# Kernel optimization log

Measured on AMD Instinct MI355X. Metric: run time of the kernel, lower is better.

## Reference

```python
import jax, jax.numpy as jnp
import numpy as np

SAMPLES = 8    # batch of sets
N = 1024       # set size == rows of the permutation-closed index matrix
K = 16         # number of distinct weight-sharing groups
M = N // K     # columns per group per row (rectangular splits)
CI = 128       # channels_in
CO = 256       # channels_out


def setup_inputs() -> dict:
    key = jax.random.key(0)
    kx, kw = jax.random.split(key)
    x = jax.random.normal(kx, (SAMPLES, N, CI), dtype=jnp.float32)
    # weightParameter: [k, channels_out, channels_in]
    W = jax.random.normal(kw, (K, CO, CI), dtype=jnp.float32)
    # Rebuild the circulant group structure that __init__ derives from
    # running_weight_matrix: row j of `indices` is roll(base, j), so the
    # columns of group g in row j are (pos_g + j) mod N.
    base = np.repeat(np.arange(K), M)                      # indices row 0, [N]
    pos = np.stack([np.where(base == g)[0] for g in range(K)])  # [K, M]
    splits = (pos[:, None, :] + np.arange(N)[None, :, None]) % N  # [K, N, M]
    return {"x": x, "W": W, "splits": jnp.asarray(splits, jnp.int32)}


def reference(x, W, splits):
    # sum-pool branch: result = sum_g ( sum_m x[:, splits[g]] ) @ W[g].T
    def body(acc, group):
        w, sp = group                      # w: [CO, CI], sp: [N, M]
        pooled = x[:, sp].sum(axis=2)      # gather [S, N, M, CI] -> [S, N, CI]
        return acc + jnp.einsum('snc,oc->sno', pooled, w), None

    init = jnp.zeros((x.shape[0], splits.shape[1], W.shape[1]), dtype=x.dtype)
    out, _ = jax.lax.scan(body, init, (W, splits))
    return out                             # [S, N, CO]
```

## Files before the change

kernel.cpp:

```cpp
#include <hip/hip_runtime.h>
#include <hip/hip_bf16.h>

#define S_   8
#define N_   1024
#define KG_  16
#define MW_  64
#define CI_  128
#define CO_  256

typedef __attribute__((ext_vector_type(8))) short bf16x8;
typedef __attribute__((ext_vector_type(4))) float f32x4;

__global__ __launch_bounds__(256) void win_kernel(const float* __restrict__ x,
                                                  const float* __restrict__ W,
                                                  __hip_bfloat16* __restrict__ win,
                                                  __hip_bfloat16* __restrict__ Wb) {
    __shared__ float lds[96][CI_];
    const int b   = blockIdx.x;
    const int tid = threadIdx.x;

    {
        const int wi = (b * 256 + tid) * 8;
        const float4 v0 = *(const float4*)&W[wi];
        const float4 v1 = *(const float4*)&W[wi + 4];
        union { unsigned short u[8]; uint4 v; } o;
        __hip_bfloat16 h;
        h = __float2bfloat16(v0.x); o.u[0] = *(unsigned short*)&h;
        h = __float2bfloat16(v0.y); o.u[1] = *(unsigned short*)&h;
        h = __float2bfloat16(v0.z); o.u[2] = *(unsigned short*)&h;
        h = __float2bfloat16(v0.w); o.u[3] = *(unsigned short*)&h;
        h = __float2bfloat16(v1.x); o.u[4] = *(unsigned short*)&h;
        h = __float2bfloat16(v1.y); o.u[5] = *(unsigned short*)&h;
        h = __float2bfloat16(v1.z); o.u[6] = *(unsigned short*)&h;
        h = __float2bfloat16(v1.w); o.u[7] = *(unsigned short*)&h;
        *(uint4*)&Wb[wi] = o.v;
    }

    const int s   = b >> 5;
    const int t0  = (b & 31) << 5;
    const float* xs = x + (size_t)s * N_ * CI_;

    for (int e = tid * 4; e < 96 * CI_; e += 256 * 4) {
        const int r = e >> 7;
        const int c = e & (CI_ - 1);
        *(float4*)&lds[r][c] = *(const float4*)&xs[((t0 + r) & (N_ - 1)) * CI_ + c];
    }
    __syncthreads();

    const int c  = tid & (CI_ - 1);
    const int tb = (tid >> 7) << 4;
    float s0 = 0.f, s1 = 0.f, s2 = 0.f, s3 = 0.f;
    #pragma unroll
    for (int m = 0; m < MW_; m += 4) {
        s0 += lds[tb + m + 0][c];
        s1 += lds[tb + m + 1][c];
        s2 += lds[tb + m + 2][c];
        s3 += lds[tb + m + 3][c];
    }
    float w = (s0 + s1) + (s2 + s3);
    __hip_bfloat16* wo = win + (size_t)s * N_ * CI_;
    wo[(t0 + tb) * CI_ + c] = __float2bfloat16(w);
    #pragma unroll
    for (int t = 1; t < 16; ++t) {
        w += lds[tb + t - 1 + MW_][c] - lds[tb + t - 1][c];
        wo[(t0 + tb + t) * CI_ + c] = __float2bfloat16(w);
    }
}

__global__ __launch_bounds__(256, 2) void gemm_kernel(const __hip_bfloat16* __restrict__ winb,
                                                      const __hip_bfloat16* __restrict__ Wb,
                                                      float* __restrict__ out) {
    __shared__ __align__(16) float red[4][64][68];

    const int tid = threadIdx.x;
    const int l   = tid & 63;
    const int wv  = tid >> 6;
    const int s   = blockIdx.x & 7;
    const int rem = blockIdx.x >> 3;
    const int n0  = (rem & 15) << 6;
    const int o0  = (rem >> 4) << 6;

    const int fr  = l & 15;
    const int kq  = l >> 4;
    const int kq8 = kq * 8;
    const int w4  = wv << 2;

    const unsigned short* winp = (const unsigned short*)winb + (size_t)s * N_ * CI_;
    const unsigned short* Wp   = (const unsigned short*)Wb;

    f32x4 acc[4][4];
    #pragma unroll
    for (int i = 0; i < 4; ++i)
        #pragma unroll
        for (int j = 0; j < 4; ++j)
            acc[i][j] = f32x4{0.f, 0.f, 0.f, 0.f};

    auto load_step = [&](int t, bf16x8* a, bf16x8* b) {
        const int g    = w4 + (t >> 2);
        const int koff = ((t & 3) << 5) + kq8;
        const int nb   = n0 + (g << 6) + fr;
        #pragma unroll
        for (int i = 0; i < 4; ++i) {
            const int row = (nb + i * 16) & (N_ - 1);
            a[i] = *(const bf16x8*)&winp[row * CI_ + koff];
        }
        const unsigned short* wg = Wp + ((g * CO_ + o0 + fr) * CI_) + koff;
        #pragma unroll
        for (int j = 0; j < 4; ++j)
            b[j] = *(const bf16x8*)&wg[j * 16 * CI_];
    };

    bf16x8 A[4][4], B[4][4];
    #pragma unroll
    for (int p = 0; p < 4; ++p) load_step(p, A[p], B[p]);

    for (int base = 0; base < 12; base += 4) {
        #pragma unroll
        for (int p = 0; p < 4; ++p) {
            #pragma unroll
            for (int i = 0; i < 4; ++i)
                #pragma unroll
                for (int j = 0; j < 4; ++j)
                    acc[i][j] = __builtin_amdgcn_mfma_f32_16x16x32_bf16(A[p][i], B[p][j], acc[i][j], 0, 0, 0);
            load_step(base + 4 + p, A[p], B[p]);
        }
    }
    #pragma unroll
    for (int p = 0; p < 4; ++p)
        #pragma unroll
        for (int i = 0; i < 4; ++i)
            #pragma unroll
            for (int j = 0; j < 4; ++j)
                acc[i][j] = __builtin_amdgcn_mfma_f32_16x16x32_bf16(A[p][i], B[p][j], acc[i][j], 0, 0, 0);

    #pragma unroll
    for (int i = 0; i < 4; ++i)
        #pragma unroll
        for (int j = 0; j < 4; ++j)
            #pragma unroll
            for (int r = 0; r < 4; ++r)
                red[wv][i * 16 + kq * 4 + r][j * 16 + fr] = acc[i][j][r];

    __syncthreads();

    const int r  = tid >> 2;
    const int cb = (tid & 3) << 4;
    float* op = out + ((size_t)(s * N_ + n0 + r) * CO_) + o0 + cb;
    #pragma unroll
    for (int q = 0; q < 4; ++q) {
        const f32x4 v0 = *(const f32x4*)&red[0][r][cb + q * 4];
        const f32x4 v1 = *(const f32x4*)&red[1][r][cb + q * 4];
        const f32x4 v2 = *(const f32x4*)&red[2][r][cb + q * 4];
        const f32x4 v3 = *(const f32x4*)&red[3][r][cb + q * 4];
        const f32x4 v  = (v0 + v1) + (v2 + v3);
        *(f32x4*)&op[q * 4] = v;
    }
}

extern "C" void kernel_launch(void* const* d_in, const int* in_sizes, int n_in,
                              void* d_out, int out_size, void* d_ws, size_t ws_size,
                              hipStream_t stream) {
    const float* x = (const float*)d_in[0];
    const float* W = (const float*)d_in[1];

    __hip_bfloat16* winb = (__hip_bfloat16*)d_ws;
    __hip_bfloat16* Wbb  = (__hip_bfloat16*)((char*)d_ws +
                              (size_t)S_ * N_ * CI_ * sizeof(__hip_bfloat16));
    float* out = (float*)d_out;

    win_kernel<<<256, 256, 0, stream>>>(x, W, winb, Wbb);
    gemm_kernel<<<512, 256, 0, stream>>>(winb, Wbb, out);
}
```

Before: 98.50 us.

## Duplicate window sums to remove modulo wrap and double-buffer GEMM loads

The window kernel now writes every pooled row twice, at row and row+N, so the GEMM can address the circular rows linearly with constant offsets instead of masking each row index. The GEMM main loop is rewritten as a fully unrolled ping-pong over two register sets of A/B fragments, with precomputed base pointers and immediate offsets. This cuts address arithmetic and register pressure compared with the four-deep register buffer. In exchange the window kernel does twice the bf16 stores and the workspace doubles, and the prefetch depth drops from four steps to two.

Result: no change. 99.21 us (+0.7%).

```diff
diff --git a/kernel.cpp b/kernel.cpp
--- a/kernel.cpp
+++ b/kernel.cpp
@@ -58,12 +58,20 @@
         s3 += lds[tb + m + 3][c];
     }
     float w = (s0 + s1) + (s2 + s3);
-    __hip_bfloat16* wo = win + (size_t)s * N_ * CI_;
-    wo[(t0 + tb) * CI_ + c] = __float2bfloat16(w);
+    __hip_bfloat16* wo = win + (size_t)s * (2 * N_) * CI_;
+    {
+        const int row = t0 + tb;
+        const __hip_bfloat16 hv = __float2bfloat16(w);
+        wo[row * CI_ + c] = hv;
+        wo[(row + N_) * CI_ + c] = hv;
+    }
     #pragma unroll
     for (int t = 1; t < 16; ++t) {
         w += lds[tb + t - 1 + MW_][c] - lds[tb + t - 1][c];
-        wo[(t0 + tb + t) * CI_ + c] = __float2bfloat16(w);
+        const int row = t0 + tb + t;
+        const __hip_bfloat16 hv = __float2bfloat16(w);
+        wo[row * CI_ + c] = hv;
+        wo[(row + N_) * CI_ + c] = hv;
     }
 }
 
@@ -82,64 +90,71 @@
 
     const int fr  = l & 15;
     const int kq  = l >> 4;
-    const int kq8 = kq * 8;
-    const int w4  = wv << 2;
 
-    const unsigned short* winp = (const unsigned short*)winb + (size_t)s * N_ * CI_;
-    const unsigned short* Wp   = (const unsigned short*)Wb;
+    const unsigned short* Ab = (const unsigned short*)winb
+        + ((size_t)s * 2 * N_ + (size_t)(n0 + (wv << 2) * MW_ + fr)) * CI_ + kq * 8;
+    const unsigned short* Bb = (const unsigned short*)Wb
+        + ((size_t)((wv << 2) * CO_ + o0 + fr)) * CI_ + kq * 8;
 
-    f32x4 acc[4][4];
-    #pragma unroll
-    for (int i = 0; i < 4; ++i)
-        #pragma unroll
-        for (int j = 0; j < 4; ++j)
-            acc[i][j] = f32x4{0.f, 0.f, 0.f, 0.f};
+#define AOFF(T,i) (((((T) >> 2) * MW_) + ((i) * 16)) * CI_ + (((T) & 3) * 32))
+#define BOFF(T,j) (((((T) >> 2) * CO_) + ((j) * 16)) * CI_ + (((T) & 3) * 32))
 
-    auto load_step = [&](int t, bf16x8* a, bf16x8* b) {
-        const int g    = w4 + (t >> 2);
-        const int koff = ((t & 3) << 5) + kq8;
-        const int nb   = n0 + (g << 6) + fr;
-        #pragma unroll
-        for (int i = 0; i < 4; ++i) {
-            const int row = (nb + i * 16) & (N_ - 1);
-            a[i] = *(const bf16x8*)&winp[row * CI_ + koff];
-        }
-        const unsigned short* wg = Wp + ((g * CO_ + o0 + fr) * CI_) + koff;
-        #pragma unroll
-        for (int j = 0; j < 4; ++j)
-            b[j] = *(const bf16x8*)&wg[j * 16 * CI_];
-    };
+    f32x4 c00 = {0.f,0.f,0.f,0.f}, c01 = {0.f,0.f,0.f,0.f}, c02 = {0.f,0.f,0.f,0.f}, c03 = {0.f,0.f,0.f,0.f};
+    f32x4 c10 = {0.f,0.f,0.f,0.f}, c11 = {0.f,0.f,0.f,0.f}, c12 = {0.f,0.f,0.f,0.f}, c13 = {0.f,0.f,0.f,0.f};
+    f32x4 c20 = {0.f,0.f,0.f,0.f}, c21 = {0.f,0.f,0.f,0.f}, c22 = {0.f,0.f,0.f,0.f}, c23 = {0.f,0.f,0.f,0.f};
+    f32x4 c30 = {0.f,0.f,0.f,0.f}, c31 = {0.f,0.f,0.f,0.f}, c32 = {0.f,0.f,0.f,0.f}, c33 = {0.f,0.f,0.f,0.f};
 
-    bf16x8 A[4][4], B[4][4];
-    #pragma unroll
-    for (int p = 0; p < 4; ++p) load_step(p, A[p], B[p]);
+    bf16x8 pa0, pa1, pa2, pa3, pb0, pb1, pb2, pb3;
+    bf16x8 qa0, qa1, qa2, qa3, qb0, qb1, qb2, qb3;
 
-    for (int base = 0; base < 12; base += 4) {
-        #pragma unroll
-        for (int p = 0; p < 4; ++p) {
-            #pragma unroll
-            for (int i = 0; i < 4; ++i)
-                #pragma unroll
-                for (int j = 0; j < 4; ++j)
-                    acc[i][j] = __builtin_amdgcn_mfma_f32_16x16x32_bf16(A[p][i], B[p][j], acc[i][j], 0, 0, 0);
-            load_step(base + 4 + p, A[p], B[p]);
-        }
-    }
-    #pragma unroll
-    for (int p = 0; p < 4; ++p)
-        #pragma unroll
-        for (int i = 0; i < 4; ++i)
-            #pragma unroll
-            for (int j = 0; j < 4; ++j)
-                acc[i][j] = __builtin_amdgcn_mfma_f32_16x16x32_bf16(A[p][i], B[p][j], acc[i][j], 0, 0, 0);
+#define LOADSET(T, S) \
+    S##a0 = *(const bf16x8*)(Ab + AOFF(T,0)); \
+    S##a1 = *(const bf16x8*)(Ab + AOFF(T,1)); \
+    S##a2 = *(const bf16x8*)(Ab + AOFF(T,2)); \
+    S##a3 = *(const bf16x8*)(Ab + AOFF(T,3)); \
+    S##b0 = *(const bf16x8*)(Bb + BOFF(T,0)); \
+    S##b1 = *(const bf16x8*)(Bb + BOFF(T,1)); \
+    S##b2 = *(const bf16x8*)(Bb + BOFF(T,2)); \
+    S##b3 = *(const bf16x8*)(Bb + BOFF(T,3));
 
-    #pragma unroll
-    for (int i = 0; i < 4; ++i)
-        #pragma unroll
-        for (int j = 0; j < 4; ++j)
-            #pragma unroll
-            for (int r = 0; r < 4; ++r)
-                red[wv][i * 16 + kq * 4 + r][j * 16 + fr] = acc[i][j][r];
+#define MM(A, B, C) C = __builtin_amdgcn_mfma_f32_16x16x32_bf16(A, B, C, 0, 0, 0)
+
+#define COMPUTESET(S) \
+    MM(S##a0, S##b0, c00); MM(S##a0, S##b1, c01); MM(S##a0, S##b2, c02); MM(S##a0, S##b3, c03); \
+    MM(S##a1, S##b0, c10); MM(S##a1, S##b1, c11); MM(S##a1, S##b2, c12); MM(S##a1, S##b3, c13); \
+    MM(S##a2, S##b0, c20); MM(S##a2, S##b1, c21); MM(S##a2, S##b2, c22); MM(S##a2, S##b3, c23); \
+    MM(S##a3, S##b0, c30); MM(S##a3, S##b1, c31); MM(S##a3, S##b2, c32); MM(S##a3, S##b3, c33);
+
+    LOADSET(0, p)
+    LOADSET(1, q)
+
+    COMPUTESET(p) LOADSET(2,  p)
+    COMPUTESET(q) LOADSET(3,  q)
+    COMPUTESET(p) LOADSET(4,  p)
+    COMPUTESET(q) LOADSET(5,  q)
+    COMPUTESET(p) LOADSET(6,  p)
+    COMPUTESET(q) LOADSET(7,  q)
+    COMPUTESET(p) LOADSET(8,  p)
+    COMPUTESET(q) LOADSET(9,  q)
+    COMPUTESET(p) LOADSET(10, p)
+    COMPUTESET(q) LOADSET(11, q)
+    COMPUTESET(p) LOADSET(12, p)
+    COMPUTESET(q) LOADSET(13, q)
+    COMPUTESET(p) LOADSET(14, p)
+    COMPUTESET(q) LOADSET(15, q)
+    COMPUTESET(p)
+    COMPUTESET(q)
+
+#define STACC(C, i, j) \
+    red[wv][(i)*16 + kq*4 + 0][(j)*16 + fr] = C[0]; \
+    red[wv][(i)*16 + kq*4 + 1][(j)*16 + fr] = C[1]; \
+    red[wv][(i)*16 + kq*4 + 2][(j)*16 + fr] = C[2]; \
+    red[wv][(i)*16 + kq*4 + 3][(j)*16 + fr] = C[3];
+
+    STACC(c00,0,0) STACC(c01,0,1) STACC(c02,0,2) STACC(c03,0,3)
+    STACC(c10,1,0) STACC(c11,1,1) STACC(c12,1,2) STACC(c13,1,3)
+    STACC(c20,2,0) STACC(c21,2,1) STACC(c22,2,2) STACC(c23,2,3)
+    STACC(c30,3,0) STACC(c31,3,1) STACC(c32,3,2) STACC(c33,3,3)
 
     __syncthreads();
 
@@ -147,13 +162,13 @@
     const int cb = (tid & 3) << 4;
     float* op = out + ((size_t)(s * N_ + n0 + r) * CO_) + o0 + cb;
     #pragma unroll
-    for (int q = 0; q < 4; ++q) {
-        const f32x4 v0 = *(const f32x4*)&red[0][r][cb + q * 4];
-        const f32x4 v1 = *(const f32x4*)&red[1][r][cb + q * 4];
-        const f32x4 v2 = *(const f32x4*)&red[2][r][cb + q * 4];
-        const f32x4 v3 = *(const f32x4*)&red[3][r][cb + q * 4];
+    for (int q2 = 0; q2 < 4; ++q2) {
+        const f32x4 v0 = *(const f32x4*)&red[0][r][cb + q2 * 4];
+        const f32x4 v1 = *(const f32x4*)&red[1][r][cb + q2 * 4];
+        const f32x4 v2 = *(const f32x4*)&red[2][r][cb + q2 * 4];
+        const f32x4 v3 = *(const f32x4*)&red[3][r][cb + q2 * 4];
         const f32x4 v  = (v0 + v1) + (v2 + v3);
-        *(f32x4*)&op[q * 4] = v;
+        *(f32x4*)&op[q2 * 4] = v;
     }
 }
 
@@ -165,7 +180,7 @@
 
     __hip_bfloat16* winb = (__hip_bfloat16*)d_ws;
     __hip_bfloat16* Wbb  = (__hip_bfloat16*)((char*)d_ws +
-                              (size_t)S_ * N_ * CI_ * sizeof(__hip_bfloat16));
+                              (size_t)S_ * 2 * N_ * CI_ * sizeof(__hip_bfloat16));
     float* out = (float*)d_out;
 
     win_kernel<<<256, 256, 0, stream>>>(x, W, winb, Wbb);
```
